# Performance work log

Hardware: AMD Instinct MI355X
Metric: run time of the kernel (lower is better)

## Reference

```python
import jax, jax.numpy as jnp
import numpy as np

B, C, L = 8, 256, 2048      # batch, res_channels, seq_len
E = 2 * C                    # attention / S4 width = 512
CH = 4                       # S4 channels
SQRT_HALF = 0.7071067811865476


def setup_inputs() -> dict:
    key = jax.random.key(0)
    ks = jax.random.split(key, 12)
    def n(k, s, sc):
        return jax.random.normal(k, s, dtype=jnp.float32) * sc
    return dict(
        x=jax.random.normal(ks[0], (B, C, L), dtype=jnp.float32),
        original=jax.random.normal(ks[1], (B, C, L), dtype=jnp.float32),
        sn_scale=jnp.ones((1, C, 1), jnp.float32),
        conv_w=n(ks[2], (E, C, 3), 0.05), conv_b=jnp.zeros((E,), jnp.float32),
        s4_ln_g=jnp.ones((E,), jnp.float32), s4_ln_b=jnp.zeros((E,), jnp.float32),
        s4_kernel=n(ks[3], (CH, E, L), 0.01),           # long-conv kernel per channel
        s4_D=n(ks[4], (CH, E), 1.0),                     # skip connection D
        s4_out_w=n(ks[5], (E, CH * E), 0.02), s4_out_b=jnp.zeros((E,), jnp.float32),
        attn_v_w=n(ks[6], (E, E), 0.02), attn_v_b=jnp.zeros((E,), jnp.float32),
        attn_o_w=n(ks[7], (E, E), 0.02), attn_o_b=jnp.zeros((E,), jnp.float32),
        res_w=n(ks[8], (C, C, 1), 0.05), res_b=jnp.zeros((C,), jnp.float32),
        skip_w=n(ks[9], (C, C, 1), 0.05), skip_b=jnp.zeros((C,), jnp.float32),
    )


def reference(x, original, sn_scale, conv_w, conv_b, s4_ln_g, s4_ln_b,
              s4_kernel, s4_D, s4_out_w, s4_out_b,
              attn_v_w, attn_v_b, attn_o_w, attn_o_b,
              res_w, res_b, skip_w, skip_b):
    eps = 1e-8
    # RMSNorm over channel dim (dim=1)
    rms = jnp.sqrt(jnp.sum(x * x, axis=1, keepdims=True)) / np.sqrt(x.shape[1]).astype(np.float32)
    x_n = sn_scale * x / (rms + eps)
    # h = x + original (pre-norm x), conv k=3 pad=1, GELU
    h = x + original
    h = jax.lax.conv_general_dilated(h, conv_w, (1,), [(1, 1)],
                                     dimension_numbers=('NCH', 'OIH', 'NCH'))
    h = jax.nn.gelu(h + conv_b[None, :, None], approximate=False)
    # --- S4 / GConv: LN over channels, FFT causal long conv, D-skip, GELU, out linear ---
    mu = h.mean(axis=1, keepdims=True)
    var = h.var(axis=1, keepdims=True)
    u = (h - mu) / jnp.sqrt(var + 1e-5) * s4_ln_g[None, :, None] + s4_ln_b[None, :, None]
    n2 = 2 * u.shape[-1]
    uf = jnp.fft.rfft(u, n=n2)                      # (B, E, F)
    kf = jnp.fft.rfft(s4_kernel, n=n2)              # (CH, E, F)
    y = jnp.fft.irfft(jnp.einsum('bhf,chf->bchf', uf, kf), n=n2)[..., :u.shape[-1]]
    y = y + s4_D[None, :, :, None] * u[:, None]     # (B, CH, E, L)
    y = jax.nn.gelu(y.reshape(y.shape[0], CH * E, y.shape[-1]), approximate=False)
    h_t = jnp.einsum('oc,bcl->bol', s4_out_w, y) + s4_out_b[None, :, None]  # (B, E, L)
    # --- local-window MHA with window_size=1: each position attends only to itself,
    # softmax over a single unmasked score == 1, so out = Wo @ (Wv @ x + bv) + bo exactly ---
    v = jnp.einsum('oe,bel->bol', attn_v_w, h_t) + attn_v_b[None, :, None]
    h_s = jnp.einsum('oe,bel->bol', attn_o_w, v) + attn_o_b[None, :, None]
    h2 = h_t + h_s
    out = jnp.tanh(h2[:, :C]) * jax.nn.sigmoid(h2[:, C:])
    res = jnp.einsum('oc,bcl->bol', res_w[:, :, 0], out) + res_b[None, :, None]
    skip = jnp.einsum('oc,bcl->bol', skip_w[:, :, 0], out) + skip_b[None, :, None]
    return ((x_n + res) * SQRT_HALF, skip)
```

## Files before the change

### kernel.cpp

```cpp
#include <hip/hip_runtime.h>
#include <hip/hip_bf16.h>
#include <math.h>

typedef __attribute__((ext_vector_type(8))) short short8;
typedef __attribute__((ext_vector_type(4))) float float4_t;
typedef __attribute__((ext_vector_type(2))) float cf2;
typedef unsigned short ushort_t;
typedef unsigned int uint_t;

#define NBL 16384

#define WS_CONVA   ((size_t)0)
#define WS_WV      ((size_t)786432)
#define WS_WO      ((size_t)1310720)
#define WS_W1      ((size_t)1835008)
#define WS_WCAT    ((size_t)3932160)
#define WS_A2      ((size_t)4194304)
#define WS_ACOMB   ((size_t)4718592)
#define WS_BCOMB   ((size_t)6815744)
#define WS_XN      ((size_t)6819840)
#define WS_H0PT    ((size_t)23597056)
#define WS_U       ((size_t)31993856)
#define WS_UF      ((size_t)65548288)
#define WS_KF      ((size_t)99102720)
#define WS_GTF     ((size_t)132657152)
#define WS_GATET   ((size_t)199766016)
#define WS_UB      ((size_t)208162816)

__device__ __forceinline__ float gelu_f(float x) {
    float t = x * x;
    float a2 = x * fmaf(0.07135481627f, t, 1.59576912161f);
    return x / (1.f + __expf(-a2));
}
__device__ __forceinline__ float tanh_f(float a) {
    return 1.f - 2.f / (1.f + __expf(2.f * a));
}
__device__ __forceinline__ float sigmoid_f(float b) {
    return 1.f / (1.f + __expf(-b));
}

__device__ __forceinline__ unsigned int pack_bf2(float a, float b) {
#if __has_builtin(__builtin_amdgcn_cvt_pk_bf16_f32)
    auto v = __builtin_amdgcn_cvt_pk_bf16_f32(a, b);
    unsigned int r; __builtin_memcpy(&r, &v, 4); return r;
#else
    __hip_bfloat16 ha = __float2bfloat16(a), hb = __float2bfloat16(b);
    unsigned short ua = *(unsigned short*)&ha, ub = *(unsigned short*)&hb;
    return (unsigned int)ua | ((unsigned int)ub << 16);
#endif
}
__device__ __forceinline__ ushort_t f2bfu(float a) {
    __hip_bfloat16 h = __float2bfloat16(a);
    return *(ushort_t*)&h;
}
__device__ __forceinline__ cf2 unpack_c(unsigned int v) {
    cf2 r;
    r.x = __uint_as_float(v << 16);
    r.y = __uint_as_float(v & 0xffff0000u);
    return r;
}
__device__ __forceinline__ float bf2f(ushort_t u) {
    return __uint_as_float(((unsigned int)u) << 16);
}

__device__ __forceinline__ void cp16(const ushort_t* g, ushort_t* l) {
    __builtin_amdgcn_global_load_lds(
        (__attribute__((address_space(1))) void*)(void*)g,
        (__attribute__((address_space(3))) void*)l, 16, 0, 0);
}

__device__ __forceinline__ cf2 cswap(cf2 a) { return __builtin_shufflevector(a, a, 1, 0); }
template<int SGN>
__device__ __forceinline__ cf2 cmuli(cf2 a) {
    cf2 s = cswap(a);
    return s * cf2{(float)(-SGN), (float)SGN};
}
__device__ __forceinline__ cf2 cmul(cf2 a, cf2 b) {
    cf2 t = cswap(a) * cf2{-b.y, b.y};
    return a * cf2{b.x, b.x} + t;
}
__device__ __forceinline__ cf2 cmulc(cf2 a, float wr, float wi) {
    cf2 t = cswap(a) * cf2{-wi, wi};
    return a * cf2{wr, wr} + t;
}

__global__ __launch_bounds__(256) void wprep_kernel(
    const float* __restrict__ conv_w, const float* __restrict__ attn_v_w,
    const float* __restrict__ attn_o_w, const float* __restrict__ s4_out_w,
    const float* __restrict__ res_w, const float* __restrict__ skip_w,
    __hip_bfloat16* __restrict__ convA, __hip_bfloat16* __restrict__ WvT,
    __hip_bfloat16* __restrict__ WoBf, __hip_bfloat16* __restrict__ W1T,
    __hip_bfloat16* __restrict__ Wcat)
{
    const int N0 = 393216, N1 = 655360, N2c = 917504, N3 = 1966080, N4 = 2097152;
    for (int i = blockIdx.x * 256 + threadIdx.x; i < N4; i += gridDim.x * 256) {
        if (i < N0) {
            int m = i / 768, r = i - m * 768, dk = r >> 8, c = r & 255;
            convA[i] = __float2bfloat16(conv_w[m * 768 + c * 3 + dk]);
        } else if (i < N1) {
            int j = i - N0; int row = j >> 9, e = j & 511;
            WvT[j] = __float2bfloat16(attn_v_w[e * 512 + row]);
        } else if (i < N2c) {
            WoBf[i - N1] = __float2bfloat16(attn_o_w[i - N1]);
        } else if (i < N3) {
            int j = i - N2c; int ck = j >> 9, e = j & 511;
            W1T[j] = __float2bfloat16(s4_out_w[e * 2048 + ck]);
        } else {
            int j = i - N3; int m = j >> 8, c = j & 255;
            float v = (m < 256) ? res_w[m * 256 + c] : skip_w[(m - 256) * 256 + c];
            Wcat[j] = __float2bfloat16(v);
        }
    }
}

__global__ __launch_bounds__(256) void bias2_kernel(
    const __hip_bfloat16* __restrict__ A2, const float* __restrict__ s4_out_b,
    const float* __restrict__ attn_o_w, const float* __restrict__ attn_v_b,
    const float* __restrict__ attn_o_b, float* __restrict__ bcomb)
{
    __shared__ float red[256];
    int o = blockIdx.x, t = threadIdx.x;
    float s = 0.f;
    for (int e = t; e < 512; e += 256)
        s += __bfloat162float(A2[o * 512 + e]) * s4_out_b[e] + attn_o_w[o * 512 + e] * attn_v_b[e];
    red[t] = s; __syncthreads();
    for (int k = 128; k > 0; k >>= 1) { if (t < k) red[t] += red[t + k]; __syncthreads(); }
    if (t == 0) bcomb[o] = red[0] + attn_o_b[o];
}

__global__ __launch_bounds__(512) void prep_kernel(
    const float* __restrict__ x, const float* __restrict__ orig,
    const float* __restrict__ sn, ushort_t* __restrict__ xnb, ushort_t* __restrict__ h0pT)
{
    __shared__ float red[8][64];
    __shared__ ushort_t T[256 * 66];
    int blk = blockIdx.x, t = threadIdx.x;
    int lane = t & 63, cg = t >> 6;
    int b = blk >> 5, l0 = (blk & 31) << 6;
    size_t basein = (size_t)b * 524288 + l0 + lane;
    float ss = 0.f;
    for (int c = cg; c < 256; c += 8) {
        size_t idx = basein + (size_t)c * 2048;
        float xv = x[idx], ov = orig[idx];
        ss += xv * xv;
        T[c * 66 + lane] = f2bfu(xv + ov);
    }
    red[cg][lane] = ss;
    __syncthreads();
    float tot = 0.f;
    #pragma unroll
    for (int k = 0; k < 8; ++k) tot += red[k][lane];
    float inv = 1.0f / (sqrtf(tot) * 0.0625f + 1e-8f);
    __hip_bfloat16* xo = (__hip_bfloat16*)xnb;
    for (int c = cg; c < 256; c += 8) {
        size_t idx = basein + (size_t)c * 2048;
        xo[idx] = __float2bfloat16(sn[c] * x[idx] * inv);
    }
    int c2 = t & 255, half = t >> 8;
    size_t rowbase = (size_t)(b * 2050 + 1 + l0);
    for (int r = half; r < 64; r += 2)
        h0pT[(rowbase + r) * 256 + c2] = T[c2 * 66 + r];
    if ((blk & 31) == 0) {
        if (t < 256) h0pT[(size_t)(b * 2050) * 256 + t] = 0;
        else         h0pT[(size_t)(b * 2050 + 2049) * 256 + (t - 256)] = 0;
    }
}

__global__ __launch_bounds__(512) void ln_kernel(
    const ushort_t* __restrict__ h, ushort_t* __restrict__ ub,
    const float* __restrict__ gam, const float* __restrict__ bet)
{
    __shared__ float r1[8][64], r2[8][64];
    int blk = blockIdx.x, t = threadIdx.x;
    int lane = t & 63, og = t >> 6;
    int n = (blk << 6) + lane;
    float s1 = 0.f, s2 = 0.f;
    for (int o = og; o < 512; o += 8) { float v = bf2f(h[(size_t)o * NBL + n]); s1 += v; s2 += v * v; }
    r1[og][lane] = s1; r2[og][lane] = s2;
    __syncthreads();
    float mu = 0.f, m2 = 0.f;
    #pragma unroll
    for (int k = 0; k < 8; ++k) { mu += r1[k][lane]; m2 += r2[k][lane]; }
    mu *= (1.f / 512.f); m2 *= (1.f / 512.f);
    float rstd = rsqrtf(m2 - mu * mu + 1e-5f);
    int b = n >> 11, l = n & 2047;
    size_t sbase = (size_t)(b >> 1) * 4096 + 2 * l + (b & 1);
    for (int o = og; o < 512; o += 8) {
        size_t idx = (size_t)o * NBL + n;
        ub[(size_t)o * 16384 + sbase] = f2bfu((bf2f(h[idx]) - mu) * rstd * gam[o] + bet[o]);
    }
}

#define PERM(m) ((((m) & 3) << 2) | ((m) >> 2))

template<int SGN>
__device__ __forceinline__ void dft4p(cf2& a0, cf2& a1, cf2& a2, cf2& a3) {
    cf2 t0 = a0 + a2, t1 = a0 - a2, t2 = a1 + a3, t3 = a1 - a3;
    cf2 j3 = cmuli<SGN>(t3);
    a0 = t0 + t2; a2 = t0 - t2;
    a1 = t1 + j3; a3 = t1 - j3;
}
template<int SGN>
__device__ __forceinline__ void dft4p_half(cf2& a0, cf2& a1, cf2& a2, cf2& a3) {
    cf2 u0 = a0, u1 = a1;
    cf2 j1 = cmuli<SGN>(u1);
    a0 = u0 + u1; a2 = u0 - u1;
    a1 = u0 + j1; a3 = u0 - j1;
}
template<int SGN>
__device__ __forceinline__ void dft4p_out01(cf2 a0, cf2 a1, cf2 a2, cf2 a3, cf2& o0, cf2& o1) {
    cf2 t0 = a0 + a2, t1 = a0 - a2, t2 = a1 + a3, t3 = a1 - a3;
    o0 = t0 + t2;
    o1 = t1 + cmuli<SGN>(t3);
}

template<int SGN>
__device__ __forceinline__ void dft16_stepB(cf2* x) {
    const float sg = (float)SGN;
    const float C16[10] = {1.f, 0.92387953f, 0.70710678f, 0.38268343f, 0.f,
                           -0.38268343f, -0.70710678f, -0.92387953f, -1.f, -0.92387953f};
    const float S16[10] = {0.f, 0.38268343f, 0.70710678f, 0.92387953f, 1.f,
                           0.92387953f, 0.70710678f, 0.38268343f, 0.f, -0.38268343f};
    #pragma unroll
    for (int s = 1; s < 4; ++s)
        #pragma unroll
        for (int r = 1; r < 4; ++r) {
            int e = s * r;
            x[4 * s + r] = cmulc(x[4 * s + r], C16[e], sg * S16[e]);
        }
}
template<int SGN>
__device__ __forceinline__ void dft16p(cf2* x) {
    #pragma unroll
    for (int r = 0; r < 4; ++r) dft4p<SGN>(x[r], x[4 + r], x[8 + r], x[12 + r]);
    dft16_stepB<SGN>(x);
    #pragma unroll
    for (int s = 0; s < 4; ++s) dft4p<SGN>(x[4 * s], x[4 * s + 1], x[4 * s + 2], x[4 * s + 3]);
}
template<int SGN>
__device__ __forceinline__ void dft16_halfin(cf2* x) {
    #pragma unroll
    for (int r = 0; r < 4; ++r) dft4p_half<SGN>(x[r], x[4 + r], x[8 + r], x[12 + r]);
    dft16_stepB<SGN>(x);
    #pragma unroll
    for (int s = 0; s < 4; ++s) dft4p<SGN>(x[4 * s], x[4 * s + 1], x[4 * s + 2], x[4 * s + 3]);
}
template<int SGN>
__device__ __forceinline__ void dft16_halfout(cf2* x, cf2* y) {
    #pragma unroll
    for (int r = 0; r < 4; ++r) dft4p<SGN>(x[r], x[4 + r], x[8 + r], x[12 + r]);
    dft16_stepB<SGN>(x);
    #pragma unroll
    for (int s = 0; s < 4; ++s)
        dft4p_out01<SGN>(x[4 * s], x[4 * s + 1], x[4 * s + 2], x[4 * s + 3], y[s], y[4 + s]);
}

template<int SGN>
__device__ __forceinline__ void tw_gen(cf2* w, float p, float invQ) {
    float s1, c1; __sincosf((float)SGN * 6.283185307179586f * p * invQ, &s1, &c1);
    w[1]  = cf2{c1, s1};
    w[2]  = cmul(w[1], w[1]);
    w[3]  = cmul(w[2], w[1]);
    w[4]  = cmul(w[2], w[2]);
    w[5]  = cmul(w[3], w[2]);
    w[6]  = cmul(w[3], w[3]);
    w[7]  = cmul(w[4], w[3]);
    w[8]  = cmul(w[4], w[4]);
    w[9]  = cmul(w[5], w[4]);
    w[10] = cmul(w[5], w[5]);
    w[11] = cmul(w[6], w[5]);
    w[12] = cmul(w[6], w[6]);
    w[13] = cmul(w[7], w[6]);
    w[14] = cmul(w[7], w[7]);
    w[15] = cmul(w[8], w[7]);
}
template<int SGN>
__device__ __forceinline__ void tw_after(cf2* x, float p, float invQ) {
    cf2 w[16];
    tw_gen<SGN>(w, p, invQ);
    #pragma unroll
    for (int m = 1; m < 16; ++m) x[PERM(m)] = cmul(x[PERM(m)], w[m]);
}
template<int SGN>
__device__ __forceinline__ void tw_before(cf2* x, float p, float invQ) {
    cf2 w[16];
    tw_gen<SGN>(w, p, invQ);
    #pragma unroll
    for (int j = 1; j < 16; ++j) x[j] = cmul(x[j], w[j]);
}

__global__ __launch_bounds__(256, 5) void fft_fwd_kernel(
    const ushort_t* __restrict__ ubf, const float* __restrict__ s4k,
    uint4* __restrict__ uf, uint4* __restrict__ kf)
{
    __shared__ cf2 S[4096];
    int wg = blockIdx.x, t = threadIdx.x;
    int tc = t >> 4, td = t & 15;
    int base = tc << 8;
    cf2 x[16];
    if (wg < 2048) {
        int bp = wg >> 9, e = wg & 511;
        const unsigned int* p0 = (const unsigned int*)ubf + (size_t)e * 8192 + (size_t)bp * 2048;
        #pragma unroll
        for (int j = 0; j < 8; ++j) x[j] = unpack_c(p0[j * 256 + t]);
    } else {
        const float* p0 = s4k + (size_t)(wg - 2048) * 2048;
        #pragma unroll
        for (int j = 0; j < 8; ++j) x[j] = cf2{p0[j * 256 + t], 0.f};
    }
    dft16_halfin<-1>(x);
    tw_after<-1>(x, (float)t, 1.f / 4096.f);
    int s1 = (tc << 4) + (tc ^ td);
    #pragma unroll
    for (int m = 0; m < 16; ++m) S[(m << 8) + s1] = x[PERM(m)];
    __syncthreads();
    #pragma unroll
    for (int j = 0; j < 16; ++j) x[j] = S[base + (j << 4) + (j ^ td)];
    dft16p<-1>(x);
    tw_after<-1>(x, (float)td, 1.f / 256.f);
    #pragma unroll
    for (int m = 0; m < 16; ++m) S[base + (m << 4) + (m ^ td)] = x[PERM(m)];
    __syncthreads();
    int b2r = base + (td << 4);
    #pragma unroll
    for (int j = 0; j < 16; ++j) x[j] = S[b2r + (td ^ j)];
    dft16p<-1>(x);
    const float sc = (wg < 2048) ? 1.f : (1.f / 4096.f);
    uint4* dst = ((wg < 2048) ? (uf + (size_t)wg * 1024) : (kf + (size_t)(wg - 2048) * 1024)) + 4 * t;
    #pragma unroll
    for (int q = 0; q < 4; ++q) {
        uint4 o;
        cf2 v0 = x[PERM(4 * q)] * sc, v1 = x[PERM(4 * q + 1)] * sc;
        cf2 v2 = x[PERM(4 * q + 2)] * sc, v3 = x[PERM(4 * q + 3)] * sc;
        o.x = pack_bf2(v0.x, v0.y);
        o.y = pack_bf2(v1.x, v1.y);
        o.z = pack_bf2(v2.x, v2.y);
        o.w = pack_bf2(v3.x, v3.y);
        dst[q] = o;
    }
}

__global__ __launch_bounds__(256) void fft_inv_kernel(
    const uint4* __restrict__ uf, const uint4* __restrict__ kf,
    const unsigned int* __restrict__ ub2, const float* __restrict__ s4D,
    ushort_t* __restrict__ gT)
{
    __shared__ cf2 S[4368];
    int bid = blockIdx.x, t = threadIdx.x;
    int tau = (bid & 7) * 1024 + (bid >> 3);
    int e = tau >> 4, ch = (tau >> 2) & 3, bp = tau & 3;
    int r = ch * 512 + e;
    const uint4* zr = uf + (size_t)(bp * 512 + e) * 1024 + 4 * t;
    const uint4* kr = kf + (size_t)(ch * 512 + e) * 1024 + 4 * t;
    cf2 x[16];
    #pragma unroll
    for (int q = 0; q < 4; ++q) {
        uint4 a4 = zr[q], b4 = kr[q];
        x[4 * q + 0] = cmul(unpack_c(a4.x), unpack_c(b4.x));
        x[4 * q + 1] = cmul(unpack_c(a4.y), unpack_c(b4.y));
        x[4 * q + 2] = cmul(unpack_c(a4.z), unpack_c(b4.z));
        x[4 * q + 3] = cmul(unpack_c(a4.w), unpack_c(b4.w));
    }
    dft16p<1>(x);
    int b1 = 273 * (t >> 4) + 17 * (t & 15);
    #pragma unroll
    for (int m = 0; m < 16; ++m) S[b1 + m] = x[PERM(m)];
    __syncthreads();
    int b2 = 273 * (t >> 4) + (t & 15);
    #pragma unroll
    for (int j = 0; j < 16; ++j) x[j] = S[b2 + 17 * j];
    tw_before<1>(x, (float)(t & 15), 1.f / 256.f);
    dft16p<1>(x);
    #pragma unroll
    for (int m = 0; m < 16; ++m) S[b2 + 17 * m] = x[PERM(m)];
    __syncthreads();
    int b3 = 17 * (t >> 4) + (t & 15);
    #pragma unroll
    for (int j = 0; j < 16; ++j) x[j] = S[b3 + 273 * j];
    tw_before<1>(x, (float)t, 1.f / 4096.f);
    cf2 y[8];
    dft16_halfout<1>(x, y);

    const float d = s4D[r];
    const unsigned int* ur = ub2 + (size_t)e * 8192 + (size_t)bp * 2048 + t;
    const size_t rpart = (size_t)(r >> 5) * 524288 + (size_t)(((r >> 3) & 3) * 128 + (r & 7));
    #pragma unroll
    for (int m = 0; m < 8; ++m) {
        int l = m * 256 + t;
        cf2 u2 = unpack_c(ur[m * 256]);
        float v0 = gelu_f(fmaf(d, u2.x, y[m].x));
        float v1 = gelu_f(fmaf(d, u2.y, y[m].y));
        int n_lo = bp * 4096 + l;
        size_t npart = (size_t)(n_lo >> 6) * 2048 + (size_t)(((n_lo >> 4) & 3) * 512 + (n_lo & 15) * 8);
        gT[rpart + npart]         = f2bfu(v0);
        gT[rpart + npart + 65536] = f2bfu(v1);
    }
}

__global__ __launch_bounds__(256) void gemmF_kernel(
    const ushort_t* __restrict__ Af, const ushort_t* __restrict__ Bf,
    ushort_t* __restrict__ Cb, const float* __restrict__ bias)
{
    __shared__ ushort_t SM[8704];
    const int t = threadIdx.x;
    const int w = t >> 6, lane = t & 63, quad = lane >> 4, lr = lane & 15;
    const int wm = (w >> 1) * 64;
    const int by = blockIdx.y, n0 = blockIdx.x * 128;
    const int h = (w >> 1) ? (4 + by) : by;
    const int nb = (n0 >> 6) + (w & 1);

    const ushort_t* Aw = Af + (size_t)h * 2048 + (size_t)lane * 8;
    const ushort_t* Bw = Bf + (size_t)nb * 2048 + (size_t)lane * 8;

    float4_t acc[4][4];
    #pragma unroll
    for (int i = 0; i < 4; ++i)
        #pragma unroll
        for (int j = 0; j < 4; ++j) { float4_t z = {0.f, 0.f, 0.f, 0.f}; acc[i][j] = z; }

    short8 a0[4], a1[4], b0[4], b1[4];

#define LDA(D, S) do { _Pragma("unroll") for (int i_ = 0; i_ < 4; ++i_) \
        D[i_] = *(const short8*)(Aw + (size_t)(S) * 16384 + i_ * 512); } while (0)
#define LDB(D, S) do { _Pragma("unroll") for (int i_ = 0; i_ < 4; ++i_) \
        D[i_] = *(const short8*)(Bw + (size_t)(S) * 524288 + i_ * 512); } while (0)
#define CMP(AA, BB) do { _Pragma("unroll") for (int im_ = 0; im_ < 4; ++im_) \
        _Pragma("unroll") for (int in_ = 0; in_ < 4; ++in_) \
            acc[im_][in_] = __builtin_amdgcn_mfma_f32_16x16x32_bf16(AA[im_], BB[in_], acc[im_][in_], 0, 0, 0); } while (0)

    LDA(a0, 0); LDB(b0, 0);
    LDA(a1, 1); LDB(b1, 1);
    for (int s = 0; s < 64; s += 2) {
        CMP(a0, b0);
        if (s + 2 < 64) { LDA(a0, s + 2); LDB(b0, s + 2); }
        CMP(a1, b1);
        if (s + 3 < 64) { LDA(a1, s + 3); LDB(b1, s + 3); }
    }
#undef LDA
#undef LDB
#undef CMP

    #pragma unroll
    for (int p = 0; p < 2; ++p) {
        if (p) __syncthreads();
        if ((w & 1) == p) {
            #pragma unroll
            for (int im = 0; im < 4; ++im)
                #pragma unroll
                for (int in_ = 0; in_ < 4; ++in_) {
                    int nl = in_ * 16 + lr;
                    #pragma unroll
                    for (int r = 0; r < 4; ++r) {
                        int i = wm + im * 16 + quad * 4 + r;
                        int me = (i < 64) ? (64 * by + i) : (192 + 64 * by + i);
                        SM[i * 68 + nl] = f2bfu(acc[im][in_][r] + bias[me]);
                    }
                }
        }
        __syncthreads();
        int nl = t >> 2, gcb = (t & 3) * 16;
        size_t obase = (size_t)(n0 + 64 * p + nl) * 256 + 64 * by + gcb;
        short8 o0, o1;
        #pragma unroll
        for (int j = 0; j < 16; ++j) {
            int gc = gcb + j;
            float a = bf2f(SM[gc * 68 + nl]);
            float bb = bf2f(SM[(gc + 64) * 68 + nl]);
            ushort_t gv = f2bfu(tanh_f(a) * sigmoid_f(bb));
            if (j < 8) o0[j] = (short)gv; else o1[j - 8] = (short)gv;
        }
        *(short8*)(Cb + obase) = o0;
        *(short8*)(Cb + obase + 8) = o1;
    }
}

template<int BSRC, int EPI>
__global__ __launch_bounds__(256, 4) void gemm_kernel(
    const ushort_t* __restrict__ A, const ushort_t* __restrict__ Bm,
    ushort_t* __restrict__ Cb, float* __restrict__ Cf,
    int M, int N, int K,
    const float* __restrict__ bias, const float* __restrict__ bias2,
    const ushort_t* __restrict__ xnb, float* __restrict__ dout)
{
    __shared__ ushort_t SM[16384];
    const int t = threadIdx.x;
    const int n0 = blockIdx.x * 64, m0 = blockIdx.y * 128;
    const int w = t >> 6, lane = t & 63, quad = lane >> 4, lr = lane & 15;
    const int wm = (w >> 1) * 64, wn = (w & 1) * 32;

    const int srow = lane >> 2;
    const int swslot = ((lane & 3) ^ ((lane >> 3) & 3)) * 8;
    const int r0q = w * 32 + srow;
    int ar0 = m0 + r0q, ar1 = m0 + r0q + 16;
    const ushort_t* aSrc0 = A + (size_t)ar0 * K + swslot;
    const ushort_t* aSrc1 = A + (size_t)ar1 * K + swslot;
    const int nrow = n0 + w * 16 + srow;
    const ushort_t* bSrc;
    if (BSRC == 0) bSrc = Bm + (size_t)nrow * K + swslot;
    else           bSrc = Bm + (size_t)((nrow >> 11) * 2050 + (nrow & 2047)) * 256 + swslot;

    const int aD = w * 1024;
    const int bD = 4096 + w * 512;

    float4_t acc[4][2];
    #pragma unroll
    for (int i = 0; i < 4; ++i)
        #pragma unroll
        for (int j = 0; j < 2; ++j) { float4_t z = {0.f, 0.f, 0.f, 0.f}; acc[i][j] = z; }

    const int qsw = (quad ^ ((lr >> 1) & 3)) << 3;

#define STAGE(BUF, KK) do {                                                     \
        cp16(aSrc0 + (KK), SM + (BUF) + aD);                                    \
        cp16(aSrc1 + (KK), SM + (BUF) + aD + 512);                              \
        if (BSRC == 0) cp16(bSrc + (KK), SM + (BUF) + bD);                      \
        else cp16(bSrc + (((KK) >> 8) * 256 + ((KK) & 255)), SM + (BUF) + bD);  \
    } while (0)

#define COMPUTE(BUF) do {                                                       \
        const ushort_t* Al = SM + (BUF);                                        \
        const ushort_t* Bl = SM + (BUF) + 4096;                                 \
        short8 af[4], bfr[2];                                                   \
        _Pragma("unroll")                                                       \
        for (int im = 0; im < 4; ++im)                                          \
            af[im] = *(const short8*)&Al[(wm + im * 16 + lr) * 32 + qsw];       \
        _Pragma("unroll")                                                       \
        for (int in_ = 0; in_ < 2; ++in_)                                       \
            bfr[in_] = *(const short8*)&Bl[(wn + in_ * 16 + lr) * 32 + qsw];    \
        _Pragma("unroll")                                                       \
        for (int im = 0; im < 4; ++im)                                          \
            _Pragma("unroll")                                                   \
            for (int in_ = 0; in_ < 2; ++in_)                                   \
                acc[im][in_] = __builtin_amdgcn_mfma_f32_16x16x32_bf16(         \
                    af[im], bfr[in_], acc[im][in_], 0, 0, 0);                   \
    } while (0)

    STAGE(0, 0);
    __syncthreads();

    for (int kt = 0; kt < K; kt += 64) {
        STAGE(8192, kt + 32);
        COMPUTE(0);
        __syncthreads();
        if (kt + 64 < K) STAGE(0, kt + 64);
        COMPUTE(8192);
        __syncthreads();
    }
#undef STAGE
#undef COMPUTE

    #pragma unroll
    for (int im = 0; im < 4; ++im) {
        #pragma unroll
        for (int in_ = 0; in_ < 2; ++in_) {
            int n = n0 + wn + in_ * 16 + lr;
            int mb = m0 + wm + im * 16 + quad * 4;
            #pragma unroll
            for (int r = 0; r < 4; ++r) {
                int m = mb + r;
                float v = acc[im][in_][r];
                if (EPI == 0) {
                    v += bias[m];
                    ((__hip_bfloat16*)Cb)[(size_t)m * N + n] = __float2bfloat16(gelu_f(v));
                } else if (EPI == 1) {
                    v += (m == n) ? 1.0f : 0.0f;
                    ((__hip_bfloat16*)Cb)[(size_t)m * N + n] = __float2bfloat16(v);
                } else if (EPI == 2) {
                    size_t fi = ((((size_t)(n >> 5) * 8 + (m >> 6)) * 4 + ((m >> 4) & 3)) * 64
                                 + ((n >> 3) & 3) * 16 + (m & 15)) * 8 + (n & 7);
                    Cb[fi] = f2bfu(v);
                } else {
                    int bb = n >> 11, ll = n & 2047;
                    if (m < 256) {
                        v += bias[m];
                        int idx = (bb << 19) + (m << 11) + ll;
                        dout[idx] = (bf2f(xnb[idx]) + v) * 0.70710678118654752f;
                    } else {
                        v += bias2[m - 256];
                        dout[4194304 + (bb << 19) + ((m - 256) << 11) + ll] = v;
                    }
                }
            }
        }
    }
}

extern "C" void kernel_launch(void* const* d_in, const int* in_sizes, int n_in,
                              void* d_out, int out_size, void* d_ws, size_t ws_size,
                              hipStream_t stream)
{
    const float* x         = (const float*)d_in[0];
    const float* original  = (const float*)d_in[1];
    const float* sn_scale  = (const float*)d_in[2];
    const float* conv_w    = (const float*)d_in[3];
    const float* conv_b    = (const float*)d_in[4];
    const float* s4_ln_g   = (const float*)d_in[5];
    const float* s4_ln_b   = (const float*)d_in[6];
    const float* s4_kernel = (const float*)d_in[7];
    const float* s4_D      = (const float*)d_in[8];
    const float* s4_out_w  = (const float*)d_in[9];
    const float* s4_out_b  = (const float*)d_in[10];
    const float* attn_v_w  = (const float*)d_in[11];
    const float* attn_v_b  = (const float*)d_in[12];
    const float* attn_o_w  = (const float*)d_in[13];
    const float* attn_o_b  = (const float*)d_in[14];
    const float* res_w     = (const float*)d_in[15];
    const float* res_b     = (const float*)d_in[16];
    const float* skip_w    = (const float*)d_in[17];
    const float* skip_b    = (const float*)d_in[18];

    char* ws = (char*)d_ws;
    __hip_bfloat16* convA = (__hip_bfloat16*)(ws + WS_CONVA);
    __hip_bfloat16* WvT   = (__hip_bfloat16*)(ws + WS_WV);
    __hip_bfloat16* WoBf  = (__hip_bfloat16*)(ws + WS_WO);
    __hip_bfloat16* W1T   = (__hip_bfloat16*)(ws + WS_W1);
    __hip_bfloat16* Wcat  = (__hip_bfloat16*)(ws + WS_WCAT);
    ushort_t* A2    = (ushort_t*)(ws + WS_A2);
    ushort_t* Acomb = (ushort_t*)(ws + WS_ACOMB);
    float* bcombp  = (float*)(ws + WS_BCOMB);
    ushort_t* xnb  = (ushort_t*)(ws + WS_XN);
    ushort_t* h0pT = (ushort_t*)(ws + WS_H0PT);
    ushort_t* hP   = (ushort_t*)(ws + WS_U);
    ushort_t* ubP  = (ushort_t*)(ws + WS_UB);
    uint4* ufP = (uint4*)(ws + WS_UF);
    uint4* kfP = (uint4*)(ws + WS_KF);
    ushort_t* gT    = (ushort_t*)(ws + WS_GTF);
    ushort_t* gateT = (ushort_t*)(ws + WS_GATET);

    wprep_kernel<<<dim3(4096), dim3(256), 0, stream>>>(conv_w, attn_v_w, attn_o_w, s4_out_w,
        res_w, skip_w, convA, WvT, WoBf, W1T, Wcat);
    gemm_kernel<0, 1><<<dim3(8, 4), dim3(256), 0, stream>>>(
        (const ushort_t*)WoBf, (const ushort_t*)WvT, A2, nullptr, 512, 512, 512,
        nullptr, nullptr, nullptr, nullptr);
    bias2_kernel<<<dim3(512), dim3(256), 0, stream>>>(
        (const __hip_bfloat16*)A2, s4_out_b, attn_o_w, attn_v_b, attn_o_b, bcombp);
    gemm_kernel<0, 2><<<dim3(32, 4), dim3(256), 0, stream>>>(
        A2, (const ushort_t*)W1T, Acomb, nullptr, 512, 2048, 512,
        nullptr, nullptr, nullptr, nullptr);

    prep_kernel<<<dim3(256), dim3(512), 0, stream>>>(x, original, sn_scale, xnb, h0pT);
    gemm_kernel<1, 0><<<dim3(256, 4), dim3(256), 0, stream>>>(
        (const ushort_t*)convA, h0pT, hP, nullptr, 512, NBL, 768,
        conv_b, nullptr, nullptr, nullptr);
    ln_kernel<<<dim3(256), dim3(512), 0, stream>>>(hP, ubP, s4_ln_g, s4_ln_b);
    fft_fwd_kernel<<<dim3(4096), dim3(256), 0, stream>>>(ubP, s4_kernel, ufP, kfP);
    fft_inv_kernel<<<dim3(8192), dim3(256), 0, stream>>>(
        ufP, kfP, (const unsigned int*)ubP, s4_D, gT);
    gemmF_kernel<<<dim3(128, 4), dim3(256), 0, stream>>>(
        (const ushort_t*)Acomb, gT, gateT, bcombp);
    gemm_kernel<0, 4><<<dim3(256, 4), dim3(256), 0, stream>>>(
        (const ushort_t*)Wcat, gateT, nullptr, nullptr, 512, NBL, 256,
        res_b, skip_b, xnb, (float*)d_out);
}
```

Measured before the change: 379.6 us.

## Pre-swizzle conv GEMM operands into MFMA fragment layout and use register-streamed GEMM

The conv weights and the im2col-expanded input are now written directly in MFMA fragment order: prep_kernel emits three shifted copies per element for the k=3 taps, and wprep swizzles convA. A new gemmFC kernel loads fragments straight from global memory into registers with double buffering, skipping LDS staging, and applies bias plus GELU in its epilogue. This removes the padded h0pT buffer and the LDS traffic of the generic conv GEMM. In exchange, prep writes three times as much data with scattered 2-byte stores, and the gT buffer is reused as scratch.

New measurement: 381.5 us. About the same (+0.5%).

```diff
diff --git a/kernel.cpp b/kernel.cpp
--- a/kernel.cpp
+++ b/kernel.cpp
@@ -19,7 +19,6 @@
 #define WS_ACOMB   ((size_t)4718592)
 #define WS_BCOMB   ((size_t)6815744)
 #define WS_XN      ((size_t)6819840)
-#define WS_H0PT    ((size_t)23597056)
 #define WS_U       ((size_t)31993856)
 #define WS_UF      ((size_t)65548288)
 #define WS_KF      ((size_t)99102720)
@@ -95,8 +94,10 @@
     const int N0 = 393216, N1 = 655360, N2c = 917504, N3 = 1966080, N4 = 2097152;
     for (int i = blockIdx.x * 256 + threadIdx.x; i < N4; i += gridDim.x * 256) {
         if (i < N0) {
-            int m = i / 768, r = i - m * 768, dk = r >> 8, c = r & 255;
-            convA[i] = __float2bfloat16(conv_w[m * 768 + c * 3 + dk]);
+            int m = i / 768, k = i - m * 768, dk = k >> 8, c = k & 255;
+            size_t fi = (size_t)(((k >> 5) * 8 + (m >> 6)) * 4 + ((m >> 4) & 3)) * 512
+                        + ((k >> 3) & 3) * 128 + (m & 15) * 8 + (k & 7);
+            convA[fi] = __float2bfloat16(conv_w[m * 768 + c * 3 + dk]);
         } else if (i < N1) {
             int j = i - N0; int row = j >> 9, e = j & 511;
             WvT[j] = __float2bfloat16(attn_v_w[e * 512 + row]);
@@ -130,7 +131,7 @@
 
 __global__ __launch_bounds__(512) void prep_kernel(
     const float* __restrict__ x, const float* __restrict__ orig,
-    const float* __restrict__ sn, ushort_t* __restrict__ xnb, ushort_t* __restrict__ h0pT)
+    const float* __restrict__ sn, ushort_t* __restrict__ xnb, ushort_t* __restrict__ bfr)
 {
     __shared__ float red[8][64];
     __shared__ ushort_t T[256 * 66];
@@ -157,12 +158,27 @@
         xo[idx] = __float2bfloat16(sn[c] * x[idx] * inv);
     }
     int c2 = t & 255, half = t >> 8;
-    size_t rowbase = (size_t)(b * 2050 + 1 + l0);
-    for (int r = half; r < 64; r += 2)
-        h0pT[(rowbase + r) * 256 + c2] = T[c2 * 66 + r];
+    for (int r = half; r < 64; r += 2) {
+        ushort_t v = T[c2 * 66 + r];
+        int l = l0 + r;
+        #pragma unroll
+        for (int dk = 0; dk < 3; ++dk) {
+            int n2 = l + 1 - dk;
+            if (n2 < 0 || n2 > 2047) continue;
+            int n = (b << 11) + n2;
+            int k = (dk << 8) + c2;
+            size_t fi = (size_t)(((k >> 5) * 256 + (n >> 6)) * 4 + ((n >> 4) & 3)) * 512
+                        + (size_t)(((k >> 3) & 3) * 128 + (n & 15) * 8 + (k & 7));
+            bfr[fi] = v;
+        }
+    }
     if ((blk & 31) == 0) {
-        if (t < 256) h0pT[(size_t)(b * 2050) * 256 + t] = 0;
-        else         h0pT[(size_t)(b * 2050 + 2049) * 256 + (t - 256)] = 0;
+        int n_, k0;
+        if (t < 256) { n_ = b << 11;          k0 = t; }
+        else         { n_ = (b << 11) + 2047; k0 = 512 + (t - 256); }
+        size_t fi = (size_t)(((k0 >> 5) * 256 + (n_ >> 6)) * 4 + ((n_ >> 4) & 3)) * 512
+                    + (size_t)(((k0 >> 3) & 3) * 128 + (n_ & 15) * 8 + (k0 & 7));
+        bfr[fi] = 0;
     }
 }
 
@@ -474,6 +490,63 @@
     }
 }
 
+__global__ __launch_bounds__(256) void gemmFC_kernel(
+    const ushort_t* __restrict__ Af, const ushort_t* __restrict__ Bf,
+    ushort_t* __restrict__ Cb, const float* __restrict__ bias)
+{
+    const int t = threadIdx.x;
+    const int w = t >> 6, lane = t & 63, quad = lane >> 4, lr = lane & 15;
+    const int by = blockIdx.y, n0 = blockIdx.x * 128;
+    const int h = by * 2 + (w >> 1);
+    const int nb = (n0 >> 6) + (w & 1);
+
+    const ushort_t* Aw = Af + (size_t)h * 2048 + (size_t)lane * 8;
+    const ushort_t* Bw = Bf + (size_t)nb * 2048 + (size_t)lane * 8;
+
+    float4_t acc[4][4];
+    #pragma unroll
+    for (int i = 0; i < 4; ++i)
+        #pragma unroll
+        for (int j = 0; j < 4; ++j) { float4_t z = {0.f, 0.f, 0.f, 0.f}; acc[i][j] = z; }
+
+    short8 a0[4], a1[4], b0[4], b1[4];
+
+#define LDA(D, S) do { _Pragma("unroll") for (int i_ = 0; i_ < 4; ++i_) \
+        D[i_] = *(const short8*)(Aw + (size_t)(S) * 16384 + i_ * 512); } while (0)
+#define LDB(D, S) do { _Pragma("unroll") for (int i_ = 0; i_ < 4; ++i_) \
+        D[i_] = *(const short8*)(Bw + (size_t)(S) * 524288 + i_ * 512); } while (0)
+#define CMP(AA, BB) do { _Pragma("unroll") for (int im_ = 0; im_ < 4; ++im_) \
+        _Pragma("unroll") for (int in_ = 0; in_ < 4; ++in_) \
+            acc[im_][in_] = __builtin_amdgcn_mfma_f32_16x16x32_bf16(AA[im_], BB[in_], acc[im_][in_], 0, 0, 0); } while (0)
+
+    LDA(a0, 0); LDB(b0, 0);
+    LDA(a1, 1); LDB(b1, 1);
+    for (int s = 0; s < 24; s += 2) {
+        CMP(a0, b0);
+        if (s + 2 < 24) { LDA(a0, s + 2); LDB(b0, s + 2); }
+        CMP(a1, b1);
+        if (s + 3 < 24) { LDA(a1, s + 3); LDB(b1, s + 3); }
+    }
+#undef LDA
+#undef LDB
+#undef CMP
+
+    #pragma unroll
+    for (int im = 0; im < 4; ++im) {
+        #pragma unroll
+        for (int in_ = 0; in_ < 4; ++in_) {
+            int n = n0 + (w & 1) * 64 + in_ * 16 + lr;
+            int mb = h * 64 + im * 16 + quad * 4;
+            #pragma unroll
+            for (int r = 0; r < 4; ++r) {
+                int m = mb + r;
+                float v = acc[im][in_][r] + bias[m];
+                ((__hip_bfloat16*)Cb)[(size_t)m * NBL + n] = __float2bfloat16(gelu_f(v));
+            }
+        }
+    }
+}
+
 template<int BSRC, int EPI>
 __global__ __launch_bounds__(256, 4) void gemm_kernel(
     const ushort_t* __restrict__ A, const ushort_t* __restrict__ Bm,
@@ -495,9 +568,7 @@
     const ushort_t* aSrc0 = A + (size_t)ar0 * K + swslot;
     const ushort_t* aSrc1 = A + (size_t)ar1 * K + swslot;
     const int nrow = n0 + w * 16 + srow;
-    const ushort_t* bSrc;
-    if (BSRC == 0) bSrc = Bm + (size_t)nrow * K + swslot;
-    else           bSrc = Bm + (size_t)((nrow >> 11) * 2050 + (nrow & 2047)) * 256 + swslot;
+    const ushort_t* bSrc = Bm + (size_t)nrow * K + swslot;
 
     const int aD = w * 1024;
     const int bD = 4096 + w * 512;
@@ -513,8 +584,7 @@
 #define STAGE(BUF, KK) do {                                                     \
         cp16(aSrc0 + (KK), SM + (BUF) + aD);                                    \
         cp16(aSrc1 + (KK), SM + (BUF) + aD + 512);                              \
-        if (BSRC == 0) cp16(bSrc + (KK), SM + (BUF) + bD);                      \
-        else cp16(bSrc + (((KK) >> 8) * 256 + ((KK) & 255)), SM + (BUF) + bD);  \
+        cp16(bSrc + (KK), SM + (BUF) + bD);                                     \
     } while (0)
 
 #define COMPUTE(BUF) do {                                                       \
@@ -559,10 +629,7 @@
             for (int r = 0; r < 4; ++r) {
                 int m = mb + r;
                 float v = acc[im][in_][r];
-                if (EPI == 0) {
-                    v += bias[m];
-                    ((__hip_bfloat16*)Cb)[(size_t)m * N + n] = __float2bfloat16(gelu_f(v));
-                } else if (EPI == 1) {
+                if (EPI == 1) {
                     v += (m == n) ? 1.0f : 0.0f;
                     ((__hip_bfloat16*)Cb)[(size_t)m * N + n] = __float2bfloat16(v);
                 } else if (EPI == 2) {
@@ -619,7 +686,6 @@
     ushort_t* Acomb = (ushort_t*)(ws + WS_ACOMB);
     float* bcombp  = (float*)(ws + WS_BCOMB);
     ushort_t* xnb  = (ushort_t*)(ws + WS_XN);
-    ushort_t* h0pT = (ushort_t*)(ws + WS_H0PT);
     ushort_t* hP   = (ushort_t*)(ws + WS_U);
     ushort_t* ubP  = (ushort_t*)(ws + WS_UB);
     uint4* ufP = (uint4*)(ws + WS_UF);
@@ -638,10 +704,9 @@
         A2, (const ushort_t*)W1T, Acomb, nullptr, 512, 2048, 512,
         nullptr, nullptr, nullptr, nullptr);
 
-    prep_kernel<<<dim3(256), dim3(512), 0, stream>>>(x, original, sn_scale, xnb, h0pT);
-    gemm_kernel<1, 0><<<dim3(256, 4), dim3(256), 0, stream>>>(
-        (const ushort_t*)convA, h0pT, hP, nullptr, 512, NBL, 768,
-        conv_b, nullptr, nullptr, nullptr);
+    prep_kernel<<<dim3(256), dim3(512), 0, stream>>>(x, original, sn_scale, xnb, gT);
+    gemmFC_kernel<<<dim3(128, 4), dim3(256), 0, stream>>>(
+        (const ushort_t*)convA, gT, hP, conv_b);
     ln_kernel<<<dim3(256), dim3(512), 0, stream>>>(hP, ubP, s4_ln_g, s4_ln_b);
     fft_fwd_kernel<<<dim3(4096), dim3(256), 0, stream>>>(ubP, s4_kernel, ufP, kfP);
     fft_inv_kernel<<<dim3(8192), dim3(256), 0, stream>>>(
```
